# Optimization experiments

Hardware: AMD Instinct MI355X
Metric: run time of the kernel (lower is better)

## Reference

```python
import jax, jax.numpy as jnp
import numpy as np

MARGIN = 0.3
NEG_FILL = -1e9


def setup_inputs() -> dict:
    key = jax.random.key(0)
    k1, k2 = jax.random.split(key)
    N, D, C = 8192, 128, 512
    features = jax.random.normal(k1, (N, D), dtype=jnp.float32)
    labels = jax.random.randint(k2, (N,), 0, C, dtype=jnp.int64)
    return {"features": features, "labels": labels}


def reference(features, labels):
    # L2-normalize rows (F.normalize default eps=1e-12)
    norm = jnp.sqrt(jnp.sum(features * features, axis=1, keepdims=True))
    f = features / jnp.maximum(norm, 1e-12)
    sim = f @ f.T                                    # [N, N]

    label_matrix = labels[:, None] == labels[None, :]  # [N, N] bool
    eye = jnp.eye(features.shape[0], dtype=bool)
    pos_mask = label_matrix & ~eye
    neg_mask = ~label_matrix

    # per-row masked mean over positives (0.0 if no positives)
    pos_cnt = jnp.sum(pos_mask, axis=1)
    pos_sum = jnp.sum(jnp.where(pos_mask, sim, 0.0), axis=1)
    pos_sim = jnp.where(pos_cnt > 0, pos_sum / jnp.maximum(pos_cnt, 1), 0.0)

    # per-row masked max over negatives (0.0 if no negatives)
    neg_any = jnp.any(neg_mask, axis=1)
    neg_max = jnp.max(jnp.where(neg_mask, sim, NEG_FILL), axis=1)
    neg_sim = jnp.where(neg_any, neg_max, 0.0)

    loss = jnp.mean(jax.nn.relu(MARGIN + neg_sim - pos_sim))
    return loss
```

## Files before the change

kernel.cpp:

```cpp
#include <hip/hip_runtime.h>
#include <hip/hip_bf16.h>

#define N_ROWS 8192
#define DIM    128
#define NCLASS 512
#define MARGIN 0.3f

typedef unsigned short u16;
typedef __attribute__((ext_vector_type(8))) short bf16x8;
typedef __attribute__((ext_vector_type(4))) float f32x4;

__device__ inline void load_lds16(const u16* g, u16* l) {
    __builtin_amdgcn_global_load_lds((const __attribute__((address_space(1))) void*)g,
                                     (__attribute__((address_space(3))) void*)l, 16, 0, 0);
}

__global__ void k_prep(const float* __restrict__ feat, float* __restrict__ fn,
                       u16* __restrict__ fb) {
    int w = threadIdx.x >> 6, lane = threadIdx.x & 63;
    int row = blockIdx.x * 4 + w;
    float2 v = *reinterpret_cast<const float2*>(feat + row * DIM + lane * 2);
    float ss = v.x * v.x + v.y * v.y;
    #pragma unroll
    for (int off = 32; off; off >>= 1) ss += __shfl_xor(ss, off);
    float r = 1.0f / fmaxf(sqrtf(ss), 1e-12f);
    float x = v.x * r, y = v.y * r;
    *reinterpret_cast<float2*>(fn + row * DIM + lane * 2) = make_float2(x, y);
    __hip_bfloat16 bx = __float2bfloat16(x), by = __float2bfloat16(y);
    u16 ux = *reinterpret_cast<u16*>(&bx), uy = *reinterpret_cast<u16*>(&by);
    ushort2 p; p.x = ux; p.y = uy;
    *reinterpret_cast<ushort2*>(fb + row * DIM + lane * 2) = p;
}

__global__ void k_clsum(const int* __restrict__ lab, const float* __restrict__ fn,
                        float* __restrict__ cs, int* __restrict__ hist) {
    __shared__ int s_cnt;
    __shared__ int s_idx[128];
    int t = threadIdx.x, c = blockIdx.x;
    if (t == 0) s_cnt = 0;
    __syncthreads();
    for (int q = t; q < N_ROWS / 4; q += 256) {
        int4 L = reinterpret_cast<const int4*>(lab)[q];
        if (L.x == c) { int p = atomicAdd(&s_cnt, 1); if (p < 128) s_idx[p] = q * 4 + 0; }
        if (L.y == c) { int p = atomicAdd(&s_cnt, 1); if (p < 128) s_idx[p] = q * 4 + 1; }
        if (L.z == c) { int p = atomicAdd(&s_cnt, 1); if (p < 128) s_idx[p] = q * 4 + 2; }
        if (L.w == c) { int p = atomicAdd(&s_cnt, 1); if (p < 128) s_idx[p] = q * 4 + 3; }
    }
    __syncthreads();
    if (t == 0) hist[c] = s_cnt;
    int cnt = s_cnt < 128 ? s_cnt : 128;
    if (t < DIM) {
        float a0 = 0.f, a1 = 0.f, a2 = 0.f, a3 = 0.f;
        int p = 0;
        for (; p + 4 <= cnt; p += 4) {
            a0 += fn[s_idx[p + 0] * DIM + t];
            a1 += fn[s_idx[p + 1] * DIM + t];
            a2 += fn[s_idx[p + 2] * DIM + t];
            a3 += fn[s_idx[p + 3] * DIM + t];
        }
        for (; p < cnt; ++p) a0 += fn[s_idx[p] * DIM + t];
        cs[c * DIM + t] = (a0 + a1) + (a2 + a3);
    }
}

__global__ __launch_bounds__(512, 4) void k_main(const u16* __restrict__ fb,
                                                 const int* __restrict__ lab,
                                                 float* __restrict__ nbp) {
    __shared__ u16 Bt[2][128 * 128];
    __shared__ float red[2][128];
    const int t = threadIdx.x;
    const int lane = t & 63, w = t >> 6;
    const int wr = w >> 1, wc = w & 1;
    const int i0 = blockIdx.x * 128;
    const int jbase = blockIdx.y * 512;
    const int l15 = lane & 15, l4 = lane >> 4;

    auto stage = [&](int jt, int buf) {
        const int j0 = jbase + jt * 128;
        #pragma unroll
        for (int it = 0; it < 4; ++it) {
            int q = it * 512 + t;
            int brow = q >> 4, kb = q & 15;
            load_lds16(fb + (j0 + brow) * DIM + ((kb ^ (brow & 7)) * 8),
                       &Bt[buf][q * 8]);
        }
    };

    bf16x8 a[2][4];
    #pragma unroll
    for (int m = 0; m < 2; ++m)
        #pragma unroll
        for (int ks = 0; ks < 4; ++ks)
            a[m][ks] = *reinterpret_cast<const bf16x8*>(
                fb + (i0 + wr * 32 + m * 16 + l15) * DIM + ks * 32 + l4 * 8);

    int labr[2][4];
    #pragma unroll
    for (int m = 0; m < 2; ++m)
        #pragma unroll
        for (int rg = 0; rg < 4; ++rg)
            labr[m][rg] = lab[i0 + wr * 32 + m * 16 + l4 * 4 + rg];

    float negp[2][4];
    #pragma unroll
    for (int m = 0; m < 2; ++m)
        #pragma unroll
        for (int rg = 0; rg < 4; ++rg) negp[m][rg] = -1e9f;

    stage(0, 0);
    __syncthreads();

    #pragma unroll
    for (int jt = 0; jt < 4; ++jt) {
        const int cb = jt & 1;
        if (jt < 3) stage(jt + 1, cb ^ 1);

        const int j0 = jbase + jt * 128;
        int labc[4];
        #pragma unroll
        for (int n = 0; n < 4; ++n) labc[n] = lab[j0 + wc * 64 + n * 16 + l15];

        f32x4 acc[2][4];
        #pragma unroll
        for (int m = 0; m < 2; ++m)
            #pragma unroll
            for (int n = 0; n < 4; ++n) acc[m][n] = f32x4{0.f, 0.f, 0.f, 0.f};

        __builtin_amdgcn_s_setprio(1);
        #pragma unroll
        for (int ks = 0; ks < 4; ++ks) {
            bf16x8 b[4];
            #pragma unroll
            for (int n = 0; n < 4; ++n) {
                int brow = wc * 64 + n * 16 + l15;
                int kb = ks * 4 + l4;
                b[n] = *reinterpret_cast<const bf16x8*>(
                    &Bt[cb][brow * DIM + ((kb ^ (brow & 7)) * 8)]);
            }
            #pragma unroll
            for (int m = 0; m < 2; ++m)
                #pragma unroll
                for (int n = 0; n < 4; ++n)
                    acc[m][n] = __builtin_amdgcn_mfma_f32_16x16x32_bf16(a[m][ks], b[n],
                                                                        acc[m][n], 0, 0, 0);
        }
        __builtin_amdgcn_s_setprio(0);

        #pragma unroll
        for (int m = 0; m < 2; ++m)
            #pragma unroll
            for (int n = 0; n < 4; ++n) {
                int lc = labc[n];
                #pragma unroll
                for (int rg = 0; rg < 4; ++rg) {
                    float s = acc[m][n][rg];
                    float v = (labr[m][rg] != lc) ? s : -1e9f;
                    negp[m][rg] = fmaxf(negp[m][rg], v);
                }
            }
        __syncthreads();
    }

    #pragma unroll
    for (int m = 0; m < 2; ++m)
        #pragma unroll
        for (int rg = 0; rg < 4; ++rg) {
            float v = negp[m][rg];
            v = fmaxf(v, __shfl_xor(v, 1));
            v = fmaxf(v, __shfl_xor(v, 2));
            v = fmaxf(v, __shfl_xor(v, 4));
            v = fmaxf(v, __shfl_xor(v, 8));
            negp[m][rg] = v;
        }
    if (l15 == 0) {
        #pragma unroll
        for (int m = 0; m < 2; ++m)
            #pragma unroll
            for (int rg = 0; rg < 4; ++rg)
                red[wc][wr * 32 + m * 16 + l4 * 4 + rg] = negp[m][rg];
    }
    __syncthreads();
    if (t < 128) {
        float v = fmaxf(red[0][t], red[1][t]);
        nbp[blockIdx.y * N_ROWS + i0 + t] = v;
    }
}

__global__ void k_loss(const float* __restrict__ fn, const float* __restrict__ cs,
                       const int* __restrict__ lab, const float* __restrict__ nbp,
                       const int* __restrict__ hist, float* __restrict__ lpart) {
    int t = threadIdx.x, lane = t & 63, w = t >> 6;
    int rbase = blockIdx.x * 128 + w * 32;
    int half = lane >> 5;
    int d0 = (lane & 31) * 4;
    float acc = 0.f;
    #pragma unroll
    for (int k = 0; k < 16; ++k) {
        int row = rbase + k * 2 + half;
        int c = lab[row];
        float4 x = *reinterpret_cast<const float4*>(fn + row * DIM + d0);
        float4 y = *reinterpret_cast<const float4*>(cs + c * DIM + d0);
        float s = x.x * y.x + x.y * y.y + x.z * y.z + x.w * y.w;
        s += __shfl_xor(s, 16); s += __shfl_xor(s, 8);
        s += __shfl_xor(s, 4);  s += __shfl_xor(s, 2); s += __shfl_xor(s, 1);
        if ((lane & 31) == 0) {
            float nm = -1e9f;
            #pragma unroll
            for (int jc = 0; jc < 16; ++jc)
                nm = fmaxf(nm, nbp[jc * N_ROWS + row]);
            float neg = nm > -1e8f ? nm : 0.0f;
            int cnt = hist[c] - 1;
            float pos = cnt > 0 ? (s - 1.0f) / (float)cnt : 0.0f;
            acc += fmaxf(0.0f, MARGIN + neg - pos);
        }
    }
    #pragma unroll
    for (int off = 32; off; off >>= 1) acc += __shfl_xor(acc, off);
    __shared__ float sm[4];
    if (lane == 0) sm[w] = acc;
    __syncthreads();
    if (t == 0) lpart[blockIdx.x] = (sm[0] + sm[1]) + (sm[2] + sm[3]);
}

__global__ void k_out(const float* __restrict__ lpart, float* __restrict__ out) {
    int t = threadIdx.x;
    float v = lpart[t];
    #pragma unroll
    for (int off = 32; off; off >>= 1) v += __shfl_xor(v, off);
    if (t == 0) out[0] = v * (1.0f / (float)N_ROWS);
}

extern "C" void kernel_launch(void* const* d_in, const int* in_sizes, int n_in,
                              void* d_out, int out_size, void* d_ws, size_t ws_size,
                              hipStream_t stream) {
    const float* feat = (const float*)d_in[0];
    const int* lab    = (const int*)d_in[1];
    char* ws = (char*)d_ws;
    float*    fn    = (float*)ws;
    u16*      fb    = (u16*)(ws + (4u << 20));
    float*    cs    = (float*)(ws + (6u << 20));
    float*    nbp   = (float*)(ws + (6u << 20) + (256u << 10));
    int*      hist  = (int*)(ws + (6u << 20) + (768u << 10));
    float*    lpart = (float*)(ws + (6u << 20) + (770u << 10));
    float*    out   = (float*)d_out;

    k_prep  <<<2048, 256, 0, stream>>>(feat, fn, fb);
    k_clsum <<<512,  256, 0, stream>>>(lab, fn, cs, hist);
    k_main  <<<dim3(64, 16), 512, 0, stream>>>(fb, lab, nbp);
    k_loss  <<<64,   256, 0, stream>>>(fn, cs, lab, nbp, hist, lpart);
    k_out   <<<1,    64,  0, stream>>>(lpart, out);
}
```

Before: 62.03 us.

## Exploit symmetric similarity: compute upper-triangular tiles, reduce rows and columns

The similarity matrix is symmetric, so the main kernel now launches only the 2080 upper-triangular 128x128 tiles. Each tile produces both row-wise and column-wise masked maxima of its negatives and writes them into a per-row, per-tile-column partial buffer. This roughly halves the MFMA and LDS work, but gives up the per-block double-buffered loop over four column tiles, so each block loads its B tile once with no overlap. The loss kernel is reorganised to reduce 64 partials per row with one wave per row, and the final reduction now sums 256 partials.

```diff
diff --git a/kernel.cpp b/kernel.cpp
--- a/kernel.cpp
+++ b/kernel.cpp
@@ -66,25 +66,27 @@
 __global__ __launch_bounds__(512, 4) void k_main(const u16* __restrict__ fb,
                                                  const int* __restrict__ lab,
                                                  float* __restrict__ nbp) {
-    __shared__ u16 Bt[2][128 * 128];
-    __shared__ float red[2][128];
+    __shared__ u16 Bt[128 * 128];
+    __shared__ float redr[2][128];
+    __shared__ float redc[4][128];
     const int t = threadIdx.x;
     const int lane = t & 63, w = t >> 6;
     const int wr = w >> 1, wc = w & 1;
-    const int i0 = blockIdx.x * 128;
-    const int jbase = blockIdx.y * 512;
     const int l15 = lane & 15, l4 = lane >> 4;
 
-    auto stage = [&](int jt, int buf) {
-        const int j0 = jbase + jt * 128;
-        #pragma unroll
-        for (int it = 0; it < 4; ++it) {
-            int q = it * 512 + t;
-            int brow = q >> 4, kb = q & 15;
-            load_lds16(fb + (j0 + brow) * DIM + ((kb ^ (brow & 7)) * 8),
-                       &Bt[buf][q * 8]);
-        }
-    };
+    int tt = blockIdx.x;
+    int bi = (int)((129.0f - sqrtf(16641.0f - 8.0f * (float)tt)) * 0.5f);
+    while (bi * 64 - bi * (bi - 1) / 2 > tt) --bi;
+    while ((bi + 1) * 64 - (bi + 1) * bi / 2 <= tt) ++bi;
+    const int bj = bi + (tt - (bi * 64 - bi * (bi - 1) / 2));
+    const int i0 = bi * 128, j0 = bj * 128;
+
+    #pragma unroll
+    for (int it = 0; it < 4; ++it) {
+        int q = it * 512 + t;
+        int brow = q >> 4, kb = q & 15;
+        load_lds16(fb + (j0 + brow) * DIM + ((kb ^ (brow & 7)) * 8), Bt + q * 8);
+    }
 
     bf16x8 a[2][4];
     #pragma unroll
@@ -101,65 +103,60 @@
         for (int rg = 0; rg < 4; ++rg)
             labr[m][rg] = lab[i0 + wr * 32 + m * 16 + l4 * 4 + rg];
 
-    float negp[2][4];
-    #pragma unroll
-    for (int m = 0; m < 2; ++m)
-        #pragma unroll
-        for (int rg = 0; rg < 4; ++rg) negp[m][rg] = -1e9f;
-
-    stage(0, 0);
-    __syncthreads();
-
-    #pragma unroll
-    for (int jt = 0; jt < 4; ++jt) {
-        const int cb = jt & 1;
-        if (jt < 3) stage(jt + 1, cb ^ 1);
-
-        const int j0 = jbase + jt * 128;
-        int labc[4];
-        #pragma unroll
-        for (int n = 0; n < 4; ++n) labc[n] = lab[j0 + wc * 64 + n * 16 + l15];
-
-        f32x4 acc[2][4];
+    int labc[4];
+    #pragma unroll
+    for (int n = 0; n < 4; ++n) labc[n] = lab[j0 + wc * 64 + n * 16 + l15];
+
+    __syncthreads();
+
+    f32x4 acc[2][4];
+    #pragma unroll
+    for (int m = 0; m < 2; ++m)
+        #pragma unroll
+        for (int n = 0; n < 4; ++n) acc[m][n] = f32x4{0.f, 0.f, 0.f, 0.f};
+
+    __builtin_amdgcn_s_setprio(1);
+    #pragma unroll
+    for (int ks = 0; ks < 4; ++ks) {
+        bf16x8 b[4];
+        #pragma unroll
+        for (int n = 0; n < 4; ++n) {
+            int brow = wc * 64 + n * 16 + l15;
+            int kb = ks * 4 + l4;
+            b[n] = *reinterpret_cast<const bf16x8*>(
+                Bt + brow * DIM + ((kb ^ (brow & 7)) * 8));
+        }
         #pragma unroll
         for (int m = 0; m < 2; ++m)
             #pragma unroll
-            for (int n = 0; n < 4; ++n) acc[m][n] = f32x4{0.f, 0.f, 0.f, 0.f};
-
-        __builtin_amdgcn_s_setprio(1);
-        #pragma unroll
-        for (int ks = 0; ks < 4; ++ks) {
-            bf16x8 b[4];
+            for (int n = 0; n < 4; ++n)
+                acc[m][n] = __builtin_amdgcn_mfma_f32_16x16x32_bf16(a[m][ks], b[n],
+                                                                    acc[m][n], 0, 0, 0);
+    }
+    __builtin_amdgcn_s_setprio(0);
+
+    float negp[2][4];
+    float colv[4];
+    #pragma unroll
+    for (int m = 0; m < 2; ++m)
+        #pragma unroll
+        for (int rg = 0; rg < 4; ++rg) negp[m][rg] = -1e9f;
+    #pragma unroll
+    for (int n = 0; n < 4; ++n) colv[n] = -1e9f;
+
+    #pragma unroll
+    for (int m = 0; m < 2; ++m)
+        #pragma unroll
+        for (int n = 0; n < 4; ++n) {
+            int lc = labc[n];
             #pragma unroll
-            for (int n = 0; n < 4; ++n) {
-                int brow = wc * 64 + n * 16 + l15;
-                int kb = ks * 4 + l4;
-                b[n] = *reinterpret_cast<const bf16x8*>(
-                    &Bt[cb][brow * DIM + ((kb ^ (brow & 7)) * 8)]);
+            for (int rg = 0; rg < 4; ++rg) {
+                float s = acc[m][n][rg];
+                float v = (labr[m][rg] != lc) ? s : -1e9f;
+                negp[m][rg] = fmaxf(negp[m][rg], v);
+                colv[n] = fmaxf(colv[n], v);
             }
-            #pragma unroll
-            for (int m = 0; m < 2; ++m)
-                #pragma unroll
-                for (int n = 0; n < 4; ++n)
-                    acc[m][n] = __builtin_amdgcn_mfma_f32_16x16x32_bf16(a[m][ks], b[n],
-                                                                        acc[m][n], 0, 0, 0);
-        }
-        __builtin_amdgcn_s_setprio(0);
-
-        #pragma unroll
-        for (int m = 0; m < 2; ++m)
-            #pragma unroll
-            for (int n = 0; n < 4; ++n) {
-                int lc = labc[n];
-                #pragma unroll
-                for (int rg = 0; rg < 4; ++rg) {
-                    float s = acc[m][n][rg];
-                    float v = (labr[m][rg] != lc) ? s : -1e9f;
-                    negp[m][rg] = fmaxf(negp[m][rg], v);
-                }
-            }
-        __syncthreads();
-    }
+        }
 
     #pragma unroll
     for (int m = 0; m < 2; ++m)
@@ -177,12 +174,31 @@
         for (int m = 0; m < 2; ++m)
             #pragma unroll
             for (int rg = 0; rg < 4; ++rg)
-                red[wc][wr * 32 + m * 16 + l4 * 4 + rg] = negp[m][rg];
-    }
-    __syncthreads();
+                redr[wc][wr * 32 + m * 16 + l4 * 4 + rg] = negp[m][rg];
+    }
+
+    #pragma unroll
+    for (int n = 0; n < 4; ++n) {
+        float v = colv[n];
+        v = fmaxf(v, __shfl_xor(v, 16));
+        v = fmaxf(v, __shfl_xor(v, 32));
+        colv[n] = v;
+    }
+    if (l4 == 0) {
+        #pragma unroll
+        for (int n = 0; n < 4; ++n)
+            redc[wr][wc * 64 + n * 16 + l15] = colv[n];
+    }
+    __syncthreads();
+
     if (t < 128) {
-        float v = fmaxf(red[0][t], red[1][t]);
-        nbp[blockIdx.y * N_ROWS + i0 + t] = v;
+        float rv = fmaxf(redr[0][t], redr[1][t]);
+        nbp[(i0 + t) * 64 + bj] = rv;
+        if (bi != bj) {
+            float cv = fmaxf(fmaxf(redc[0][t], redc[1][t]),
+                             fmaxf(redc[2][t], redc[3][t]));
+            nbp[(j0 + t) * 64 + bi] = cv;
+        }
     }
 }
 
@@ -190,32 +206,28 @@
                        const int* __restrict__ lab, const float* __restrict__ nbp,
                        const int* __restrict__ hist, float* __restrict__ lpart) {
     int t = threadIdx.x, lane = t & 63, w = t >> 6;
-    int rbase = blockIdx.x * 128 + w * 32;
-    int half = lane >> 5;
-    int d0 = (lane & 31) * 4;
+    int rbase = blockIdx.x * 32 + w * 8;
     float acc = 0.f;
     #pragma unroll
-    for (int k = 0; k < 16; ++k) {
-        int row = rbase + k * 2 + half;
+    for (int k = 0; k < 8; ++k) {
+        int row = rbase + k;
         int c = lab[row];
-        float4 x = *reinterpret_cast<const float4*>(fn + row * DIM + d0);
-        float4 y = *reinterpret_cast<const float4*>(cs + c * DIM + d0);
-        float s = x.x * y.x + x.y * y.y + x.z * y.z + x.w * y.w;
-        s += __shfl_xor(s, 16); s += __shfl_xor(s, 8);
-        s += __shfl_xor(s, 4);  s += __shfl_xor(s, 2); s += __shfl_xor(s, 1);
-        if ((lane & 31) == 0) {
-            float nm = -1e9f;
-            #pragma unroll
-            for (int jc = 0; jc < 16; ++jc)
-                nm = fmaxf(nm, nbp[jc * N_ROWS + row]);
+        float2 x = *reinterpret_cast<const float2*>(fn + row * DIM + lane * 2);
+        float2 y = *reinterpret_cast<const float2*>(cs + c * DIM + lane * 2);
+        float s = x.x * y.x + x.y * y.y;
+        float nm = nbp[row * 64 + lane];
+        #pragma unroll
+        for (int off = 32; off; off >>= 1) {
+            s += __shfl_xor(s, off);
+            nm = fmaxf(nm, __shfl_xor(nm, off));
+        }
+        if (lane == 0) {
             float neg = nm > -1e8f ? nm : 0.0f;
             int cnt = hist[c] - 1;
             float pos = cnt > 0 ? (s - 1.0f) / (float)cnt : 0.0f;
             acc += fmaxf(0.0f, MARGIN + neg - pos);
         }
     }
-    #pragma unroll
-    for (int off = 32; off; off >>= 1) acc += __shfl_xor(acc, off);
     __shared__ float sm[4];
     if (lane == 0) sm[w] = acc;
     __syncthreads();
@@ -224,7 +236,7 @@
 
 __global__ void k_out(const float* __restrict__ lpart, float* __restrict__ out) {
     int t = threadIdx.x;
-    float v = lpart[t];
+    float v = lpart[t] + lpart[t + 64] + lpart[t + 128] + lpart[t + 192];
     #pragma unroll
     for (int off = 32; off; off >>= 1) v += __shfl_xor(v, off);
     if (t == 0) out[0] = v * (1.0f / (float)N_ROWS);
@@ -240,13 +252,13 @@
     u16*      fb    = (u16*)(ws + (4u << 20));
     float*    cs    = (float*)(ws + (6u << 20));
     float*    nbp   = (float*)(ws + (6u << 20) + (256u << 10));
-    int*      hist  = (int*)(ws + (6u << 20) + (768u << 10));
-    float*    lpart = (float*)(ws + (6u << 20) + (770u << 10));
+    int*      hist  = (int*)(ws + (6u << 20) + (2304u << 10));
+    float*    lpart = (float*)(ws + (6u << 20) + (2306u << 10));
     float*    out   = (float*)d_out;
 
     k_prep  <<<2048, 256, 0, stream>>>(feat, fn, fb);
     k_clsum <<<512,  256, 0, stream>>>(lab, fn, cs, hist);
-    k_main  <<<dim3(64, 16), 512, 0, stream>>>(fb, lab, nbp);
-    k_loss  <<<64,   256, 0, stream>>>(fn, cs, lab, nbp, hist, lpart);
+    k_main  <<<2080, 512, 0, stream>>>(fb, lab, nbp);
+    k_loss  <<<256,  256, 0, stream>>>(fn, cs, lab, nbp, hist, lpart);
     k_out   <<<1,    64,  0, stream>>>(lpart, out);
 }
```

Measured after the change: 58.64 us. -5.5%, faster.
